# Optimization experiments

Measured on AMD Instinct MI355X. Metric: run time of the kernel, lower is better.

The kernel has to match this reference:

```python
import jax, jax.numpy as jnp
import numpy as np

B, T, D, H = 64, 512, 256, 512

def setup_inputs() -> dict:
    key = jax.random.key(0)
    ks = jax.random.split(key, 5)
    s = 1.0 / np.sqrt(D + H)  # keep gate pre-activations in a sane range
    return {
        "x": jax.random.normal(ks[0], (B, T, D), dtype=jnp.float32),
        "Wf": jax.random.normal(ks[1], (D + H, H), dtype=jnp.float32) * s,
        "bf": jnp.zeros((H,), dtype=jnp.float32),
        "Wi": jax.random.normal(ks[2], (D + H, H), dtype=jnp.float32) * s,
        "bi": jnp.zeros((H,), dtype=jnp.float32),
        "Wo": jax.random.normal(ks[3], (D + H, H), dtype=jnp.float32) * s,
        "bo": jnp.zeros((H,), dtype=jnp.float32),
        "Wc": jax.random.normal(ks[4], (D + H, H), dtype=jnp.float32) * s,
        "bc": jnp.zeros((H,), dtype=jnp.float32),
    }

def reference(x, Wf, bf, Wi, bi, Wo, bo, Wc, bc):
    # x: [B, T, D]; unidirectional LSTM, zero initial hidden/cell state.
    batch, dur, _ = x.shape
    hid = Wf.shape[1]
    h0 = jnp.zeros((batch, hid), dtype=x.dtype)
    c0 = jnp.zeros((batch, hid), dtype=x.dtype)

    def step(carry, xt):
        h, c = carry
        z = jnp.concatenate([xt, h], axis=1)  # [B, D+H]
        f = jax.nn.sigmoid(z @ Wf + bf)
        i = jax.nn.sigmoid(z @ Wi + bi)
        c_tilde = jnp.tanh(z @ Wc + bc)
        o = jax.nn.sigmoid(z @ Wo + bo)
        c_new = c * f + c_tilde * i
        h_new = o * jnp.tanh(c_new)
        return (h_new, c_new), h_new

    _, hs = jax.lax.scan(step, (h0, c0), jnp.swapaxes(x, 0, 1))  # hs: [T, B, H]
    return jnp.swapaxes(hs, 0, 1)  # [B, T, H]
```

## Files before the change

kernel.cpp:

```cpp
#include <hip/hip_runtime.h>


#define B_   64
#define T_   512
#define D_   256
#define H_   512
#define NCL  4
#define WPC  32
#define BPC  16
#define NKT  24
#define NCT  4
#define ZPAD 776

typedef __attribute__((ext_vector_type(8)))  short  short8;
typedef __attribute__((ext_vector_type(4)))  float  f32x4;
typedef __attribute__((ext_vector_type(4)))  float  float4_;
typedef unsigned short ushort_t;
typedef unsigned int   uint_t;

__device__ __forceinline__ ushort_t f2bf(float f) {
    unsigned int u = __float_as_uint(f);
    u += 0x7FFFu + ((u >> 16) & 1u);
    return (ushort_t)(u >> 16);
}
__device__ __forceinline__ float bf2f(ushort_t h) {
    return __uint_as_float(((unsigned int)h) << 16);
}
__device__ __forceinline__ float sigm_(float x) { return 1.0f / (1.0f + __expf(-x)); }
__device__ __forceinline__ float tanh_(float x) {
    float a = fabsf(x);
    float e = __expf(-2.0f * a);
    float r = (1.0f - e) / (1.0f + e);
    return copysignf(r, x);
}

__global__ __launch_bounds__(256, 1)
void lstm_persistent(const float* __restrict__ x,
                     const float* __restrict__ Wf, const float* __restrict__ bf_,
                     const float* __restrict__ Wi, const float* __restrict__ bi_,
                     const float* __restrict__ Wo, const float* __restrict__ bo_,
                     const float* __restrict__ Wc, const float* __restrict__ bc_,
                     float* __restrict__ out,
                     uint_t* __restrict__ flags,
                     uint_t* __restrict__ hpack)
{
    __shared__ ushort_t w_lds[NCT * NKT * 512];
    __shared__ ushort_t z_hi[16 * ZPAD];
    __shared__ ushort_t z_lo[16 * ZPAD];
    __shared__ float    bias_lds[64];

    const int tid  = threadIdx.x;
    const int lane = tid & 63;
    const int wv   = tid >> 6;
    const int cl   = blockIdx.x >> 5;
    const int w    = blockIdx.x & 31;
    const int b0   = cl * BPC;
    const int hc0  = w * 16;

    for (int idx = tid; idx < NCT * NKT * 64; idx += 256) {
        int blk   = idx >> 6;
        int ln    = idx & 63;
        int ct    = blk / NKT;
        int kt    = blk % NKT;
        int col16 = ln & 15;
        int kc    = ln >> 4;
        int j     = ct * 16 + col16;
        int hc    = j >> 2, g = j & 3;
        int gcol  = hc0 + hc;
        const float* Wsrc = (g == 0) ? Wf : ((g == 1) ? Wi : ((g == 2) ? Wo : Wc));
        int krow0 = kt * 32 + kc * 8;
        short8 v;
#pragma unroll
        for (int jj = 0; jj < 8; ++jj)
            v[jj] = (short)f2bf(Wsrc[(size_t)(krow0 + jj) * H_ + gcol]);
        *(short8*)(w_lds + blk * 512 + ln * 8) = v;
    }
    if (tid < 64) {
        int g = tid & 3, hc = tid >> 2;
        const float* bsrc = (g == 0) ? bf_ : ((g == 1) ? bi_ : ((g == 2) ? bo_ : bc_));
        bias_lds[tid] = bsrc[hc0 + hc];
    }
    __syncthreads();

    float c_reg = 0.0f;
    const int bx = tid & 15, ch = tid >> 4;
    const float* xbase = x + (size_t)(b0 + bx) * (T_ * D_) + ch * 16;

    float4_ xr0, xr1, xr2, xr3;
    {
        const float4_* p = (const float4_*)xbase;
        xr0 = p[0]; xr1 = p[1]; xr2 = p[2]; xr3 = p[3];
    }

    const int l15 = lane & 15, lk = lane >> 4;
    const ushort_t* zh_frag = z_hi + l15 * ZPAD + lk * 8;
    const ushort_t* zl_frag = z_lo + l15 * ZPAD + lk * 8;
    const ushort_t* wfrag   = w_lds + lane * 8;
    float* pC = (float*)z_hi;

    const int gb = tid >> 4, ghc = tid & 15;
    const int ctg = ghc >> 2;

    for (int t = 0; t < T_; ++t) {
        {
            ushort_t hp[16], lp[16];
#pragma unroll
            for (int e = 0; e < 4; ++e) {
                float xf; ushort_t hb;
                xf = xr0[e]; hb = f2bf(xf); hp[e]      = hb; lp[e]      = f2bf(xf - bf2f(hb));
                xf = xr1[e]; hb = f2bf(xf); hp[4 + e]  = hb; lp[4 + e]  = f2bf(xf - bf2f(hb));
                xf = xr2[e]; hb = f2bf(xf); hp[8 + e]  = hb; lp[8 + e]  = f2bf(xf - bf2f(hb));
                xf = xr3[e]; hb = f2bf(xf); hp[12 + e] = hb; lp[12 + e] = f2bf(xf - bf2f(hb));
            }
            short8 a0, a1, b0v, b1v;
#pragma unroll
            for (int e = 0; e < 8; ++e) {
                a0[e] = (short)hp[e]; a1[e] = (short)hp[8 + e];
                b0v[e] = (short)lp[e]; b1v[e] = (short)lp[8 + e];
            }
            ushort_t* zh = z_hi + bx * ZPAD + ch * 16;
            ushort_t* zl = z_lo + bx * ZPAD + ch * 16;
            ((short8*)zh)[0] = a0; ((short8*)zh)[1] = a1;
            ((short8*)zl)[0] = b0v; ((short8*)zl)[1] = b1v;
        }

        if (t > 0) {
            if (lane < WPC) {
                const uint_t* fl = flags + cl * WPC + lane;
                while (__hip_atomic_load(fl, __ATOMIC_RELAXED, __HIP_MEMORY_SCOPE_AGENT) < (uint_t)t)
                    __builtin_amdgcn_s_sleep(2);
            }
            __builtin_amdgcn_fence(__ATOMIC_ACQUIRE, "workgroup");
        }

        {
            const uint_t* hsrc = hpack + (size_t)((t & 1) * NCL + cl) * (BPC * H_);
            uint_t hvr[32];
#pragma unroll
            for (int q = 0; q < 32; ++q)
                hvr[q] = __hip_atomic_load(hsrc + q * 256 + tid,
                                           __ATOMIC_RELAXED, __HIP_MEMORY_SCOPE_AGENT);
#pragma unroll
            for (int q = 0; q < 32; ++q) {
                int zo = (q >> 1) * ZPAD + 256 + (q & 1) * 256 + tid;
                z_hi[zo] = (ushort_t)(hvr[q] >> 16);
                z_lo[zo] = (ushort_t)(hvr[q] & 0xffffu);
            }
        }
        __syncthreads();

        if (t + 1 < T_) {
            const float4_* p = (const float4_*)(xbase + (size_t)(t + 1) * D_);
            xr0 = p[0]; xr1 = p[1]; xr2 = p[2]; xr3 = p[3];
        }

        f32x4 acc0 = {0.f, 0.f, 0.f, 0.f};
        f32x4 acc1 = {0.f, 0.f, 0.f, 0.f};
        f32x4 acc2 = {0.f, 0.f, 0.f, 0.f};
        f32x4 acc3 = {0.f, 0.f, 0.f, 0.f};
        const int kt0 = wv * 6;
#pragma unroll
        for (int k6 = 0; k6 < 6; ++k6) {
            const int kt = kt0 + k6;
            short8 ah = *(const short8*)(zh_frag + kt * 32);
            short8 al = *(const short8*)(zl_frag + kt * 32);
            short8 bb;
            bb = *(const short8*)(wfrag + (0 * NKT + kt) * 512);
            acc0 = __builtin_amdgcn_mfma_f32_16x16x32_bf16(ah, bb, acc0, 0, 0, 0);
            acc0 = __builtin_amdgcn_mfma_f32_16x16x32_bf16(al, bb, acc0, 0, 0, 0);
            bb = *(const short8*)(wfrag + (1 * NKT + kt) * 512);
            acc1 = __builtin_amdgcn_mfma_f32_16x16x32_bf16(ah, bb, acc1, 0, 0, 0);
            acc1 = __builtin_amdgcn_mfma_f32_16x16x32_bf16(al, bb, acc1, 0, 0, 0);
            bb = *(const short8*)(wfrag + (2 * NKT + kt) * 512);
            acc2 = __builtin_amdgcn_mfma_f32_16x16x32_bf16(ah, bb, acc2, 0, 0, 0);
            acc2 = __builtin_amdgcn_mfma_f32_16x16x32_bf16(al, bb, acc2, 0, 0, 0);
            bb = *(const short8*)(wfrag + (3 * NKT + kt) * 512);
            acc3 = __builtin_amdgcn_mfma_f32_16x16x32_bf16(ah, bb, acc3, 0, 0, 0);
            acc3 = __builtin_amdgcn_mfma_f32_16x16x32_bf16(al, bb, acc3, 0, 0, 0);
        }
        __syncthreads();

#pragma unroll
        for (int i = 0; i < 4; ++i) {
            int r = (lk * 4 + i) * 16 + l15;
            pC[(wv * 4 + 0) * 256 + r] = acc0[i];
            pC[(wv * 4 + 1) * 256 + r] = acc1[i];
            pC[(wv * 4 + 2) * 256 + r] = acc2[i];
            pC[(wv * 4 + 3) * 256 + r] = acc3[i];
        }
        __syncthreads();

        float hout;
        {
            float pre[4];
#pragma unroll
            for (int g = 0; g < 4; ++g) {
                float s = bias_lds[ghc * 4 + g];
                const int col = (ghc & 3) * 4 + g;
#pragma unroll
                for (int wv2 = 0; wv2 < 4; ++wv2)
                    s += pC[(wv2 * 4 + ctg) * 256 + gb * 16 + col];
                pre[g] = s;
            }
            float fg = sigm_(pre[0]);
            float ig = sigm_(pre[1]);
            float og = sigm_(pre[2]);
            float cc = tanh_(pre[3]);
            c_reg = fmaf(c_reg, fg, cc * ig);
            hout = og * tanh_(c_reg);

            uint_t hb = (uint_t)f2bf(hout);
            uint_t lb = (uint_t)f2bf(hout - bf2f((ushort_t)hb));
            size_t ho = (size_t)(((t + 1) & 1) * NCL + cl) * (BPC * H_)
                      + (size_t)gb * H_ + hc0 + ghc;
            __hip_atomic_store(hpack + ho, (hb << 16) | lb,
                               __ATOMIC_RELAXED, __HIP_MEMORY_SCOPE_AGENT);
        }

        asm volatile("s_waitcnt vmcnt(0)" ::: "memory");
        __syncthreads();

        if (tid == 0)
            __hip_atomic_store(flags + cl * WPC + w, (uint_t)(t + 1),
                               __ATOMIC_RELAXED, __HIP_MEMORY_SCOPE_AGENT);

        out[((size_t)(b0 + gb) * T_ + t) * H_ + hc0 + ghc] = hout;
    }
}

extern "C" void kernel_launch(void* const* d_in, const int* in_sizes, int n_in,
                              void* d_out, int out_size, void* d_ws, size_t ws_size,
                              hipStream_t stream) {
    const float* x  = (const float*)d_in[0];
    const float* Wf = (const float*)d_in[1];
    const float* bf = (const float*)d_in[2];
    const float* Wi = (const float*)d_in[3];
    const float* bi = (const float*)d_in[4];
    const float* Wo = (const float*)d_in[5];
    const float* bo = (const float*)d_in[6];
    const float* Wc = (const float*)d_in[7];
    const float* bc = (const float*)d_in[8];
    float* out = (float*)d_out;

    uint_t* flags = (uint_t*)d_ws;
    uint_t* hpack = (uint_t*)((char*)d_ws + 1024);

    hipMemsetAsync(d_ws, 0, 1024 + 2 * NCL * BPC * H_ * sizeof(uint_t), stream);

    lstm_persistent<<<dim3(NCL * WPC), dim3(256), 0, stream>>>(
        x, Wf, bf, Wi, bi, Wo, bo, Wc, bc, out, flags, hpack);
}
```

Measured before the change: 1.687 ms.

## Replace flag barrier with sequence-tagged 64-bit h exchange and register-resident weights

Each h value is now stored as a 64-bit word with its timestep in the upper half. Consumers spin on those words directly, so the separate per-block flag, the vmcnt drain and the extra barrier before publishing are gone. Weight fragments are also preloaded into registers once, and the weight LDS is reused as the partial-sum scratch. This removes one __syncthreads and the LDS weight reads per step. The cost is higher register pressure (96 VGPRs of weights) and more global traffic, since h now moves as 64-bit words.

```diff
diff --git a/kernel.cpp b/kernel.cpp
--- a/kernel.cpp
+++ b/kernel.cpp
@@ -17,6 +17,7 @@
 typedef __attribute__((ext_vector_type(4)))  float  float4_;
 typedef unsigned short ushort_t;
 typedef unsigned int   uint_t;
+typedef unsigned long long u64_t;
 
 __device__ __forceinline__ ushort_t f2bf(float f) {
     unsigned int u = __float_as_uint(f);
@@ -41,8 +42,7 @@
                      const float* __restrict__ Wo, const float* __restrict__ bo_,
                      const float* __restrict__ Wc, const float* __restrict__ bc_,
                      float* __restrict__ out,
-                     uint_t* __restrict__ flags,
-                     uint_t* __restrict__ hpack)
+                     u64_t* __restrict__ hpack)
 {
     __shared__ ushort_t w_lds[NCT * NKT * 512];
     __shared__ ushort_t z_hi[16 * ZPAD];
@@ -82,6 +82,14 @@
     }
     __syncthreads();
 
+    short8 Bf[NCT][6];
+#pragma unroll
+    for (int ct = 0; ct < NCT; ++ct)
+#pragma unroll
+        for (int k6 = 0; k6 < 6; ++k6)
+            Bf[ct][k6] = *(const short8*)(w_lds + (ct * NKT + wv * 6 + k6) * 512 + lane * 8);
+    float* pC = (float*)w_lds;
+
     float c_reg = 0.0f;
     const int bx = tid & 15, ch = tid >> 4;
     const float* xbase = x + (size_t)(b0 + bx) * (T_ * D_) + ch * 16;
@@ -92,11 +100,15 @@
         xr0 = p[0]; xr1 = p[1]; xr2 = p[2]; xr3 = p[3];
     }
 
+#pragma unroll
+    for (int q = 0; q < 32; ++q) {
+        int zo = (q >> 1) * ZPAD + 256 + (q & 1) * 256 + tid;
+        z_hi[zo] = 0; z_lo[zo] = 0;
+    }
+
     const int l15 = lane & 15, lk = lane >> 4;
     const ushort_t* zh_frag = z_hi + l15 * ZPAD + lk * 8;
     const ushort_t* zl_frag = z_lo + l15 * ZPAD + lk * 8;
-    const ushort_t* wfrag   = w_lds + lane * 8;
-    float* pC = (float*)z_hi;
 
     const int gb = tid >> 4, ghc = tid & 15;
     const int ctg = ghc >> 2;
@@ -125,27 +137,26 @@
         }
 
         if (t > 0) {
-            if (lane < WPC) {
-                const uint_t* fl = flags + cl * WPC + lane;
-                while (__hip_atomic_load(fl, __ATOMIC_RELAXED, __HIP_MEMORY_SCOPE_AGENT) < (uint_t)t)
-                    __builtin_amdgcn_s_sleep(2);
-            }
-            __builtin_amdgcn_fence(__ATOMIC_ACQUIRE, "workgroup");
-        }
-
-        {
-            const uint_t* hsrc = hpack + (size_t)((t & 1) * NCL + cl) * (BPC * H_);
-            uint_t hvr[32];
-#pragma unroll
-            for (int q = 0; q < 32; ++q)
-                hvr[q] = __hip_atomic_load(hsrc + q * 256 + tid,
-                                           __ATOMIC_RELAXED, __HIP_MEMORY_SCOPE_AGENT);
-#pragma unroll
-            for (int q = 0; q < 32; ++q) {
-                int zo = (q >> 1) * ZPAD + 256 + (q & 1) * 256 + tid;
-                z_hi[zo] = (ushort_t)(hvr[q] >> 16);
-                z_lo[zo] = (ushort_t)(hvr[q] & 0xffffu);
-            }
+            const u64_t* hsrc = hpack + (size_t)((t & 1) * NCL + cl) * (BPC * H_);
+            const uint_t want = (uint_t)t;
+            uint_t mask = 0xffffffffu;
+            do {
+                u64_t v[32];
+#pragma unroll
+                for (int q = 0; q < 32; ++q)
+                    if (mask & (1u << q))
+                        v[q] = __hip_atomic_load(hsrc + q * 256 + tid,
+                                                 __ATOMIC_RELAXED, __HIP_MEMORY_SCOPE_AGENT);
+#pragma unroll
+                for (int q = 0; q < 32; ++q)
+                    if ((mask & (1u << q)) && (uint_t)(v[q] >> 32) == want) {
+                        int zo = (q >> 1) * ZPAD + 256 + (q & 1) * 256 + tid;
+                        uint_t d = (uint_t)v[q];
+                        z_hi[zo] = (ushort_t)(d >> 16);
+                        z_lo[zo] = (ushort_t)(d & 0xffffu);
+                        mask &= ~(1u << q);
+                    }
+            } while (mask);
         }
         __syncthreads();
 
@@ -164,21 +175,15 @@
             const int kt = kt0 + k6;
             short8 ah = *(const short8*)(zh_frag + kt * 32);
             short8 al = *(const short8*)(zl_frag + kt * 32);
-            short8 bb;
-            bb = *(const short8*)(wfrag + (0 * NKT + kt) * 512);
-            acc0 = __builtin_amdgcn_mfma_f32_16x16x32_bf16(ah, bb, acc0, 0, 0, 0);
-            acc0 = __builtin_amdgcn_mfma_f32_16x16x32_bf16(al, bb, acc0, 0, 0, 0);
-            bb = *(const short8*)(wfrag + (1 * NKT + kt) * 512);
-            acc1 = __builtin_amdgcn_mfma_f32_16x16x32_bf16(ah, bb, acc1, 0, 0, 0);
-            acc1 = __builtin_amdgcn_mfma_f32_16x16x32_bf16(al, bb, acc1, 0, 0, 0);
-            bb = *(const short8*)(wfrag + (2 * NKT + kt) * 512);
-            acc2 = __builtin_amdgcn_mfma_f32_16x16x32_bf16(ah, bb, acc2, 0, 0, 0);
-            acc2 = __builtin_amdgcn_mfma_f32_16x16x32_bf16(al, bb, acc2, 0, 0, 0);
-            bb = *(const short8*)(wfrag + (3 * NKT + kt) * 512);
-            acc3 = __builtin_amdgcn_mfma_f32_16x16x32_bf16(ah, bb, acc3, 0, 0, 0);
-            acc3 = __builtin_amdgcn_mfma_f32_16x16x32_bf16(al, bb, acc3, 0, 0, 0);
-        }
-        __syncthreads();
+            acc0 = __builtin_amdgcn_mfma_f32_16x16x32_bf16(ah, Bf[0][k6], acc0, 0, 0, 0);
+            acc0 = __builtin_amdgcn_mfma_f32_16x16x32_bf16(al, Bf[0][k6], acc0, 0, 0, 0);
+            acc1 = __builtin_amdgcn_mfma_f32_16x16x32_bf16(ah, Bf[1][k6], acc1, 0, 0, 0);
+            acc1 = __builtin_amdgcn_mfma_f32_16x16x32_bf16(al, Bf[1][k6], acc1, 0, 0, 0);
+            acc2 = __builtin_amdgcn_mfma_f32_16x16x32_bf16(ah, Bf[2][k6], acc2, 0, 0, 0);
+            acc2 = __builtin_amdgcn_mfma_f32_16x16x32_bf16(al, Bf[2][k6], acc2, 0, 0, 0);
+            acc3 = __builtin_amdgcn_mfma_f32_16x16x32_bf16(ah, Bf[3][k6], acc3, 0, 0, 0);
+            acc3 = __builtin_amdgcn_mfma_f32_16x16x32_bf16(al, Bf[3][k6], acc3, 0, 0, 0);
+        }
 
 #pragma unroll
         for (int i = 0; i < 4; ++i) {
@@ -211,18 +216,12 @@
 
             uint_t hb = (uint_t)f2bf(hout);
             uint_t lb = (uint_t)f2bf(hout - bf2f((ushort_t)hb));
+            u64_t pk = ((u64_t)(uint_t)(t + 1) << 32) | ((u64_t)hb << 16) | lb;
             size_t ho = (size_t)(((t + 1) & 1) * NCL + cl) * (BPC * H_)
                       + (size_t)gb * H_ + hc0 + ghc;
-            __hip_atomic_store(hpack + ho, (hb << 16) | lb,
+            __hip_atomic_store(hpack + ho, pk,
                                __ATOMIC_RELAXED, __HIP_MEMORY_SCOPE_AGENT);
         }
-
-        asm volatile("s_waitcnt vmcnt(0)" ::: "memory");
-        __syncthreads();
-
-        if (tid == 0)
-            __hip_atomic_store(flags + cl * WPC + w, (uint_t)(t + 1),
-                               __ATOMIC_RELAXED, __HIP_MEMORY_SCOPE_AGENT);
 
         out[((size_t)(b0 + gb) * T_ + t) * H_ + hc0 + ghc] = hout;
     }
@@ -242,11 +241,9 @@
     const float* bc = (const float*)d_in[8];
     float* out = (float*)d_out;
 
-    uint_t* flags = (uint_t*)d_ws;
-    uint_t* hpack = (uint_t*)((char*)d_ws + 1024);
-
-    hipMemsetAsync(d_ws, 0, 1024 + 2 * NCL * BPC * H_ * sizeof(uint_t), stream);
+    u64_t* hpack = (u64_t*)d_ws;
+    hipMemsetAsync(d_ws, 0, (size_t)2 * NCL * BPC * H_ * sizeof(u64_t), stream);
 
     lstm_persistent<<<dim3(NCL * WPC), dim3(256), 0, stream>>>(
-        x, Wf, bf, Wi, bi, Wo, bo, Wc, bc, out, flags, hpack);
-}
+        x, Wf, bf, Wi, bi, Wo, bo, Wc, bc, out, hpack);
+}
```

Result: slower. 2.582 ms (+53.0%).
